# Kernel tuning notes

Measured on AMD Instinct MI355X. Metric: run time of the kernel, lower is better.

## Reference

```python
import jax, jax.numpy as jnp
import numpy as np

DEPTH = 4
CHUNK = 16


def tp(a, b):
    """Graded tensor (outer) product on flattened levels: (...,m)x(...,n)->(...,m*n)."""
    return jnp.einsum('...i,...j->...ij', a, b).reshape(*a.shape[:-1], a.shape[-1] * b.shape[-1])


def ta_mul(a, b):
    """Truncated tensor-algebra product of two group-like elements (implicit level-0 == 1).
    a, b: lists of levels 1..D, level k flattened to C**k."""
    out = []
    for k in range(len(a)):
        t = a[k] + b[k]
        for i in range(k):
            t = t + tp(a[i], b[k - 1 - i])
        out.append(t)
    return out


def ta_mulz(a, b):
    """Product when both elements have level-0 == 0."""
    out = []
    for k in range(len(a)):
        t = jnp.zeros_like(a[k])
        for i in range(k):
            t = t + tp(a[i], b[k - 1 - i])
        out.append(t)
    return out


def ta_exp(a):
    """exp of a level-0-free element, truncated at DEPTH; returns levels 1..D (level-0 == 1 implicit)."""
    out = list(a)
    p = a
    fact = 1.0
    for m in range(2, len(a) + 1):
        p = ta_mulz(a, p)
        fact *= m
        out = [o + q / fact for o, q in zip(out, p)]
    return out


def ta_log(s):
    """Truncated log of group-like element g = 1 + s; input s = levels 1..D of g."""
    out = list(s)
    p = s
    sign = 1.0
    for m in range(2, len(s) + 1):
        p = ta_mulz(s, p)
        sign = -sign
        out = [o + (sign / m) * q for o, q in zip(out, p)]
    return out


def bch(a, b):
    """BCH merge: log(exp(a) (x) exp(b)) in the truncated algebra."""
    return ta_log(ta_mul(ta_exp(a), ta_exp(b)))


def exp_l1(d):
    """exp of a pure level-1 element d (shape (...,C)): level k = d^(x)k / k!."""
    levels = [d]
    cur = d
    fact = 1.0
    for k in range(2, DEPTH + 1):
        cur = tp(cur, d)
        fact *= k
        levels.append(cur / fact)
    return levels


def chunk_signatures(inc):
    """inc: (B, N, L, C) per-chunk increments -> signature levels [(B,N,C), (B,N,C^2), ...]
    via Chen: sig = exp(d_1) (x) ... (x) exp(d_L)."""
    carry0 = tuple(exp_l1(inc[:, :, 0]))
    xs = jnp.moveaxis(inc[:, :, 1:], 2, 0)  # (L-1, B, N, C)
    def step(carry, d):
        return tuple(ta_mul(list(carry), exp_l1(d))), None
    carry, _ = jax.lax.scan(step, carry0, xs)
    return list(carry)


def hillis_steele(levels):
    """Inclusive associative scan over chunk dim (axis=1) with BCH merge.
    bch(0, b) == b exactly, so zero-padding handles the boundary."""
    N = levels[0].shape[1]
    pref = levels
    d = 1
    while d < N:
        shifted = [jnp.concatenate([jnp.zeros_like(l[:, :d]), l[:, :-d]], axis=1) for l in pref]
        pref = bch(shifted, pref)
        d *= 2
    return pref


def _forward(x, W1, b1, W2, b2):
    B, T, Cin = x.shape
    t = jnp.linspace(0.0, 1.0, T, dtype=x.dtype)
    path = jnp.concatenate([x, jnp.broadcast_to(t[None, :, None], (B, T, 1)).astype(x.dtype)], axis=-1)
    C = Cin + 1
    # basepoint=True: path starts at 0, so increments are diff of [0; path]
    inc = jnp.diff(path, axis=1, prepend=jnp.zeros((B, 1, C), x.dtype))
    N = T // CHUNK
    inc = inc.reshape(B, N, CHUNK, C)
    sig = chunk_signatures(inc)          # levels 1..D, (B,N,C^k)
    logl = ta_log(sig)                   # truncated log-signature per chunk
    pref = hillis_steele(logl)           # inclusive BCH prefix scan
    flat = jnp.concatenate(pref, axis=-1)  # (B, N, mem_dim)
    pooled = flat.mean(axis=1)           # readout_pool == 'mean'
    h = jnp.maximum(pooled @ W1 + b1, 0.0)
    return h @ W2 + b2


def setup_inputs() -> dict:
    key = jax.random.key(0)
    k0, k1, k2 = jax.random.split(key, 3)
    B, T, Cin = 8, 2048, 7
    mem_dim, H, out_dim = 4680, 256, 1
    x = jax.random.normal(k0, (B, T, Cin), dtype=jnp.float32)
    W1 = jax.random.normal(k1, (mem_dim, H), dtype=jnp.float32) * (1.0 / np.sqrt(mem_dim))
    b1 = jnp.zeros((H,), jnp.float32)
    W2 = jax.random.normal(k2, (H, out_dim), dtype=jnp.float32) * (1.0 / np.sqrt(H))
    b2 = jnp.zeros((out_dim,), jnp.float32)
    return {"x": x, "W1": W1, "b1": b1, "W2": W2, "b2": b2}


def reference(x, W1, b1, W2, b2):
    return _forward(x, W1, b1, W2, b2)
```

## Files before the change

### kernel.cpp

```cpp
#include <hip/hip_runtime.h>


#define MEM   4680
#define L2OFF 8
#define L3OFF 72
#define L4OFF 584
#define NG    32
#define TLEN  2048
#define ZN    (8 * MEM + 8 * 256)

__device__ __forceinline__ void load_inc(const float* __restrict__ x, int b, int g,
                                         float* sInc, int tid) {
    for (int e = tid; e < 512; e += 256) {
        int s = e >> 3, c = e & 7;
        int t = g * 64 + s;
        float v;
        if (c < 7) {
            float cur  = x[(b * TLEN + t) * 7 + c];
            float prev = (t > 0) ? x[(b * TLEN + t - 1) * 7 + c] : 0.f;
            v = cur - prev;
        } else v = (t > 0) ? (1.f / 2047.f) : 0.f;
        sInc[e] = v;
    }
}

__device__ __forceinline__ void chunk_step(const float* dch, float* sA, float* U, int tid) {
    float* loc3 = U;
    float* loc2 = U + 512;
    float* loc1 = U + 576;
    const int i1 = tid >> 6, j1 = (tid >> 3) & 7, k1 = tid & 7;
    const int pos2 = tid + 256, i2 = pos2 >> 6;
    float p1a = 0.f, l2a = 0.f, l3a = 0.f, p1b = 0.f, l2b = 0.f, l3b = 0.f;
    float Sa[8], Sb[8];
#pragma unroll
    for (int l = 0; l < 8; l++) { Sa[l] = 0.f; Sb[l] = 0.f; }
#pragma unroll
    for (int t = 0; t < 16; t++) {
        const float* dr = dch + t * 8;
        float di1 = dr[i1], di2 = dr[i2], dj = dr[j1], dk = dr[k1];
        float ga = l3a + dk * (l2a * 0.5f + dj * (p1a * (1.f/6.f) + di1 * (1.f/24.f)));
        float gb = l3b + dk * (l2b * 0.5f + dj * (p1b * (1.f/6.f) + di2 * (1.f/24.f)));
#pragma unroll
        for (int l = 0; l < 8; l++) { float dv = dr[l]; Sa[l] += ga * dv; Sb[l] += gb * dv; }
        l3a += dk * (l2a + dj * (p1a * 0.5f + di1 * (1.f/6.f)));
        l3b += dk * (l2b + dj * (p1b * 0.5f + di2 * (1.f/6.f)));
        l2a += (p1a + di1 * 0.5f) * dj;
        l2b += (p1b + di2 * 0.5f) * dj;
        p1a += di1; p1b += di2;
    }
    loc3[tid] = l3a; loc3[pos2] = l3b;
    if (k1 == 0) { loc2[tid >> 3] = l2a; loc2[(tid >> 3) + 32] = l2b; }
    if ((tid & 63) == 0) { loc1[i1] = p1a; loc1[i2] = p1b; }
    __syncthreads();
    float n4a[8], n4b[8];
    {
        float a1 = sA[i1], a2 = sA[L2OFF + (tid >> 3)], a3 = sA[L3OFF + tid];
        float c1_ = sA[i2], c2_ = sA[L2OFF + (tid >> 3) + 32], c3_ = sA[L3OFF + pos2];
        const float* l3p = &loc3[(tid & 63) * 8];
        const float* l2p = &loc2[k1 * 8];
#pragma unroll
        for (int l = 0; l < 8; l++) {
            float v3 = l3p[l], v2 = l2p[l], v1 = loc1[l];
            n4a[l] = sA[L4OFF + tid * 8 + l]  + Sa[l] + a1 * v3 + a2 * v2 + a3 * v1;
            n4b[l] = sA[L4OFF + pos2 * 8 + l] + Sb[l] + c1_ * v3 + c2_ * v2 + c3_ * v1;
        }
    }
    float n3a = sA[L3OFF + tid]  + l3a + sA[i1] * loc2[tid & 63] + sA[L2OFF + (tid >> 3)] * loc1[k1];
    float n3b = sA[L3OFF + pos2] + l3b + sA[i2] * loc2[tid & 63] + sA[L2OFF + (tid >> 3) + 32] * loc1[k1];
    float n2v = 0.f, n1v = 0.f;
    if (tid < 64) n2v = sA[L2OFF + tid] + loc2[tid] + sA[tid >> 3] * loc1[tid & 7];
    if (tid < 8)  n1v = sA[tid] + loc1[tid];
    __syncthreads();
#pragma unroll
    for (int l = 0; l < 8; l++) { sA[L4OFF + tid * 8 + l] = n4a[l]; sA[L4OFF + pos2 * 8 + l] = n4b[l]; }
    sA[L3OFF + tid] = n3a; sA[L3OFF + pos2] = n3b;
    if (tid < 64) sA[L2OFF + tid] = n2v;
    if (tid < 8)  sA[tid] = n1v;
    __syncthreads();
}

__global__ __launch_bounds__(256) void sig_totals_kernel(const float* __restrict__ x,
                                                         float* __restrict__ T,
                                                         float* __restrict__ zbuf) {
    int blk = blockIdx.x;
    int b = blk >> 5, g = blk & 31;
    int tid = threadIdx.x;

    for (int i = blk * 256 + tid; i < ZN; i += 256 * 256) zbuf[i] = 0.f;

    __shared__ __attribute__((aligned(16))) float sInc[512];
    __shared__ __attribute__((aligned(16))) float sA[MEM];
    __shared__ __attribute__((aligned(16))) float U[584];

    load_inc(x, b, g, sInc, tid);
    for (int m = tid; m < MEM; m += 256) sA[m] = 0.f;
    __syncthreads();
    for (int c = 0; c < 4; c++) chunk_step(&sInc[c * 128], sA, U, tid);
    const float4* s4 = (const float4*)sA;
    float4* t4 = (float4*)(T + (size_t)blk * MEM);
    for (int m = tid; m < MEM / 4; m += 256) t4[m] = s4[m];
}

__global__ __launch_bounds__(256) void scan_fused_kernel(const float* __restrict__ T,
                                                         float* __restrict__ P) {
    int bx = blockIdx.x;
    int b = bx >> 4, s = bx & 15;
    int tid = threadIdx.x;

    __shared__ float st1[NG][8];
    __shared__ float st2[NG][64];
    __shared__ float st3[NG][32];
    __shared__ float sp1[NG][8];
    __shared__ float sp2[NG][64];
    __shared__ float sp3[NG][32];

    int bBase = b * NG;
    {
        int g = tid >> 3, i = tid & 7;
        st1[g][i] = T[(size_t)(bBase + g) * MEM + i];
    }
    for (int m = tid; m < NG * 64; m += 256) {
        int g = m >> 6, e = m & 63;
        st2[g][e] = T[(size_t)(bBase + g) * MEM + L2OFF + e];
    }
    for (int m = tid; m < NG * 32; m += 256) {
        int g = m >> 5, e = m & 31;
        st3[g][e] = T[(size_t)(bBase + g) * MEM + L3OFF + s * 32 + e];
    }
    __syncthreads();

    if (tid < 64) {
        int i = tid >> 3, k = tid & 7;
        float p1acc = 0.f, p2acc = 0.f;
        for (int g = 0; g < NG; g++) {
            sp2[g][tid] = p2acc;
            if (k == 0) sp1[g][i] = p1acc;
            if (s == 0) {
                size_t prow = (size_t)(bBase + g) * MEM;
                P[prow + L2OFF + tid] = p2acc;
                if (k == 0) P[prow + i] = p1acc;
            }
            p2acc += st2[g][tid] + p1acc * st1[g][k];
            p1acc += st1[g][i];
        }
    }
    __syncthreads();
    if (tid < 32) {
        int ijk = s * 32 + tid;
        int i = ijk >> 6, jk = ijk & 63, ij = ijk >> 3, k = ijk & 7;
        float acc3 = 0.f;
        for (int g = 0; g < NG; g++) {
            sp3[g][tid] = acc3;
            P[(size_t)(bBase + g) * MEM + L3OFF + ijk] = acc3;
            acc3 += st3[g][tid] + sp1[g][i] * st2[g][jk] + sp2[g][ij] * st1[g][k];
        }
    }
    __syncthreads();
    {
        int m = s * 256 + tid;
        int i = m >> 9, jkl = m & 511, ij = m >> 6, kl = m & 63, l = m & 7;
        int p3loc = tid >> 3;
        float acc4 = 0.f;
#pragma unroll 4
        for (int g = 0; g < NG; g++) {
            size_t row = (size_t)(bBase + g) * MEM;
            P[row + L4OFF + m] = acc4;
            acc4 += T[row + L4OFF + m]
                  + sp1[g][i] * T[row + L3OFF + jkl]
                  + sp2[g][ij] * st2[g][kl]
                  + sp3[g][p3loc] * st1[g][l];
        }
    }
}

__global__ __launch_bounds__(256) void apply_log_pool_kernel(const float* __restrict__ x,
                                                             const float* __restrict__ P,
                                                             float* __restrict__ pooled) {
    int blk = blockIdx.x;
    int b = blk >> 5, g = blk & 31;
    int tid = threadIdx.x;

    __shared__ __attribute__((aligned(16))) float sInc[512];
    __shared__ __attribute__((aligned(16))) float sA[MEM];
    __shared__ __attribute__((aligned(16))) float sP[MEM];
    __shared__ __attribute__((aligned(16))) float U[1680];

    load_inc(x, b, g, sInc, tid);
    {
        const float4* p4 = (const float4*)(P + (size_t)blk * MEM);
        float4* sp4 = (float4*)sP;
        for (int m = tid; m < MEM / 4; m += 256) sp4[m] = p4[m];
    }
    for (int m = tid; m < MEM; m += 256) sA[m] = 0.f;
    __syncthreads();

    const int i1 = tid >> 6, j1 = (tid >> 3) & 7, k1 = tid & 7;
    const int pos2 = tid + 256, i2 = pos2 >> 6;
    float pool4a[8], pool4b[8];
#pragma unroll
    for (int l = 0; l < 8; l++) { pool4a[l] = 0.f; pool4b[l] = 0.f; }
    float pool3a = 0.f, pool3b = 0.f, pool2 = 0.f, pool1 = 0.f;
    float* sR = U + 584;
    float* sQ23 = U + 1168;

    for (int c = 0; c < 4; c++) {
        chunk_step(&sInc[c * 128], sA, U, tid);
        float R4a[8], R4b[8];
        {
            float a1 = sP[i1], a2 = sP[L2OFF + (tid >> 3)], a3 = sP[L3OFF + tid];
            float c1_ = sP[i2], c2_ = sP[L2OFF + (tid >> 3) + 32], c3_ = sP[L3OFF + pos2];
            const float* q3p = &sA[L3OFF + (tid & 63) * 8];
            const float* q2p = &sA[L2OFF + k1 * 8];
#pragma unroll
            for (int l = 0; l < 8; l++) {
                float v3 = q3p[l], v2 = q2p[l], v1 = sA[l];
                R4a[l] = sP[L4OFF + tid * 8 + l]  + sA[L4OFF + tid * 8 + l]  + a1 * v3 + a2 * v2 + a3 * v1;
                R4b[l] = sP[L4OFF + pos2 * 8 + l] + sA[L4OFF + pos2 * 8 + l] + c1_ * v3 + c2_ * v2 + c3_ * v1;
            }
        }
        float R3a = sP[L3OFF + tid]  + sA[L3OFF + tid]  + sP[i1] * sA[L2OFF + (tid & 63)] + sP[L2OFF + (tid >> 3)] * sA[k1];
        float R3b = sP[L3OFF + pos2] + sA[L3OFF + pos2] + sP[i2] * sA[L2OFF + (tid & 63)] + sP[L2OFF + (tid >> 3) + 32] * sA[k1];
        float R2v = 0.f, R1v = 0.f;
        if (tid < 64) R2v = sP[L2OFF + tid] + sA[L2OFF + tid] + sP[tid >> 3] * sA[tid & 7];
        if (tid < 8)  R1v = sP[tid] + sA[tid];
        sR[72 + tid] = R3a; sR[72 + pos2] = R3b;
        if (tid < 64) sR[8 + tid] = R2v;
        if (tid < 8)  sR[tid] = R1v;
        __syncthreads();
        sQ23[tid]  = sR[tid >> 6] * sR[8 + (tid & 63)] + sR[8 + (tid >> 3)] * sR[tid & 7];
        sQ23[pos2] = sR[pos2 >> 6] * sR[8 + (tid & 63)] + sR[8 + (tid >> 3) + 32] * sR[tid & 7];
        __syncthreads();
        {
            float s1ia = sR[i1], s1ib = sR[i2], s1j = sR[j1], s1k = sR[k1];
            float s2ija = sR[8 + (tid >> 3)], s2ijb = sR[8 + (tid >> 3) + 32];
            const float* r3p = &sR[72 + (tid & 63) * 8];
            const float* r2p = &sR[8 + k1 * 8];
            const float* q23p = &sQ23[(tid & 63) * 8];
#pragma unroll
            for (int l = 0; l < 8; l++) {
                float s1l = sR[l];
                float p22 = s1k * s1l;
                float p24a = s1ia * r3p[l] + s2ija * r2p[l] + R3a * s1l;
                float p24b = s1ib * r3p[l] + s2ijb * r2p[l] + R3b * s1l;
                float p34a = s1ia * q23p[l] + s2ija * p22;
                float p34b = s1ib * q23p[l] + s2ijb * p22;
                float p44a = s1ia * s1j * p22;
                float p44b = s1ib * s1j * p22;
                pool4a[l] += R4a[l] - 0.5f * p24a + (1.f/3.f) * p34a - 0.25f * p44a;
                pool4b[l] += R4b[l] - 0.5f * p24b + (1.f/3.f) * p34b - 0.25f * p44b;
            }
            pool3a += R3a - 0.5f * sQ23[tid]  + (1.f/3.f) * s1ia * s1j * s1k;
            pool3b += R3b - 0.5f * sQ23[pos2] + (1.f/3.f) * s1ib * s1j * s1k;
            if (tid < 64) pool2 += R2v - 0.5f * sR[tid >> 3] * sR[tid & 7];
            if (tid < 8)  pool1 += R1v;
        }
        __syncthreads();
    }
    {
        const float sc = 1.f / 128.f;
        float* pb = pooled + (size_t)b * MEM;
#pragma unroll
        for (int l = 0; l < 8; l++) {
            atomicAdd(&pb[L4OFF + tid * 8 + l],  pool4a[l] * sc);
            atomicAdd(&pb[L4OFF + pos2 * 8 + l], pool4b[l] * sc);
        }
        atomicAdd(&pb[L3OFF + tid],  pool3a * sc);
        atomicAdd(&pb[L3OFF + pos2], pool3b * sc);
        if (tid < 64) atomicAdd(&pb[L2OFF + tid], pool2 * sc);
        if (tid < 8)  atomicAdd(&pb[tid], pool1 * sc);
    }
}

__global__ __launch_bounds__(256) void gemv1_kernel(const float* __restrict__ pooled,
                                                    const float* __restrict__ W1,
                                                    float* __restrict__ hbuf) {
    int kc = blockIdx.x;
    int tid = threadIdx.x;
    int k0 = kc * 32;
    __shared__ float sp[8][32];
    {
        int b = tid >> 5, kk = tid & 31;
        sp[b][kk] = (k0 + kk < MEM) ? pooled[b * MEM + k0 + kk] : 0.f;
    }
    __syncthreads();
    float acc[8];
#pragma unroll
    for (int b = 0; b < 8; b++) acc[b] = 0.f;
    int kend = (k0 + 32 < MEM) ? (k0 + 32) : MEM;
    for (int k = k0; k < kend; k++) {
        float wv = W1[(size_t)k * 256 + tid];
#pragma unroll
        for (int b = 0; b < 8; b++) acc[b] += sp[b][k - k0] * wv;
    }
#pragma unroll
    for (int b = 0; b < 8; b++) atomicAdd(&hbuf[b * 256 + tid], acc[b]);
}

__global__ __launch_bounds__(256) void final_kernel(const float* __restrict__ hbuf,
                                                    const float* __restrict__ b1,
                                                    const float* __restrict__ W2,
                                                    const float* __restrict__ b2,
                                                    float* __restrict__ outp) {
    int b = blockIdx.x;
    int tid = threadIdx.x;
    float v = hbuf[b * 256 + tid] + b1[tid];
    v = fmaxf(v, 0.f) * W2[tid];
    __shared__ float sRed[256];
    sRed[tid] = v;
    __syncthreads();
    for (int s = 128; s > 0; s >>= 1) {
        if (tid < s) sRed[tid] += sRed[tid + s];
        __syncthreads();
    }
    if (tid == 0) outp[b] = sRed[0] + b2[0];
}

extern "C" void kernel_launch(void* const* d_in, const int* in_sizes, int n_in,
                              void* d_out, int out_size, void* d_ws, size_t ws_size,
                              hipStream_t stream) {
    const float* x  = (const float*)d_in[0];
    const float* W1 = (const float*)d_in[1];
    const float* b1 = (const float*)d_in[2];
    const float* W2 = (const float*)d_in[3];
    const float* b2 = (const float*)d_in[4];
    float* out = (float*)d_out;

    float* ws = (float*)d_ws;
    float* T      = ws;
    float* P      = T + (size_t)256 * MEM;
    float* pooled = P + (size_t)256 * MEM;
    float* hbuf   = pooled + 8 * MEM;

    sig_totals_kernel<<<256, 256, 0, stream>>>(x, T, pooled);
    scan_fused_kernel<<<128, 256, 0, stream>>>(T, P);
    apply_log_pool_kernel<<<256, 256, 0, stream>>>(x, P, pooled);
    gemv1_kernel<<<147, 256, 0, stream>>>(pooled, W1, hbuf);
    final_kernel<<<8, 256, 0, stream>>>(hbuf, b1, W2, b2, out);
}
```

Baseline: 152.0 us.

## Pad shared-memory signature rows to stride 9 and replace atomics with partial-sum buffers

Level-3 and level-4 tensors in shared memory are stored with a row stride of 9 instead of 8, so the strided per-thread accesses no longer hit the same LDS banks. The pooled reduction and the hidden-layer reduction now write per-block partial buffers, which the next kernel sums, instead of using global atomicAdd. This also removes the zero-initialisation pass. In exchange the code does extra global traffic: the 256x4680 partial buffer is read by gemv1 and 147 partial slices are summed in final_kernel. Shared memory per block also grows.

```diff
diff --git a/kernel.cpp b/kernel.cpp
--- a/kernel.cpp
+++ b/kernel.cpp
@@ -2,12 +2,12 @@
 
 
 #define MEM   4680
-#define L2OFF 8
-#define L3OFF 72
-#define L4OFF 584
 #define NG    32
 #define TLEN  2048
-#define ZN    (8 * MEM + 8 * 256)
+
+#define P3OFF 72
+#define P4OFF 648
+#define SIGSZ 5256
 
 __device__ __forceinline__ void load_inc(const float* __restrict__ x, int b, int g,
                                          float* sInc, int tid) {
@@ -26,9 +26,11 @@
 
 __device__ __forceinline__ void chunk_step(const float* dch, float* sA, float* U, int tid) {
     float* loc3 = U;
-    float* loc2 = U + 512;
-    float* loc1 = U + 576;
+    float* loc2 = U + 576;
+    float* loc1 = U + 640;
     const int i1 = tid >> 6, j1 = (tid >> 3) & 7, k1 = tid & 7;
+    const int row1 = tid >> 3, row2 = row1 + 32;
+    const int jk = tid & 63;
     const int pos2 = tid + 256, i2 = pos2 >> 6;
     float p1a = 0.f, l2a = 0.f, l3a = 0.f, p1b = 0.f, l2b = 0.f, l3b = 0.f;
     float Sa[8], Sb[8];
@@ -48,57 +50,60 @@
         l2b += (p1b + di2 * 0.5f) * dj;
         p1a += di1; p1b += di2;
     }
-    loc3[tid] = l3a; loc3[pos2] = l3b;
-    if (k1 == 0) { loc2[tid >> 3] = l2a; loc2[(tid >> 3) + 32] = l2b; }
-    if ((tid & 63) == 0) { loc1[i1] = p1a; loc1[i2] = p1b; }
-    __syncthreads();
+    loc3[row1 * 9 + k1] = l3a;
+    loc3[row2 * 9 + k1] = l3b;
+    if (k1 == 0) { loc2[row1] = l2a; loc2[row2] = l2b; }
+    if (jk == 0) { loc1[i1] = p1a; loc1[i2] = p1b; }
+    __syncthreads();
+    float a1 = sA[i1], a2 = sA[8 + row1], a3 = sA[P3OFF + row1 * 9 + k1];
+    float c1_ = sA[i2], c2_ = sA[8 + row2], c3_ = sA[P3OFF + row2 * 9 + k1];
+    const float* l3p = &loc3[jk * 9];
+    const float* l2p = &loc2[k1 * 8];
     float n4a[8], n4b[8];
-    {
-        float a1 = sA[i1], a2 = sA[L2OFF + (tid >> 3)], a3 = sA[L3OFF + tid];
-        float c1_ = sA[i2], c2_ = sA[L2OFF + (tid >> 3) + 32], c3_ = sA[L3OFF + pos2];
-        const float* l3p = &loc3[(tid & 63) * 8];
-        const float* l2p = &loc2[k1 * 8];
-#pragma unroll
-        for (int l = 0; l < 8; l++) {
-            float v3 = l3p[l], v2 = l2p[l], v1 = loc1[l];
-            n4a[l] = sA[L4OFF + tid * 8 + l]  + Sa[l] + a1 * v3 + a2 * v2 + a3 * v1;
-            n4b[l] = sA[L4OFF + pos2 * 8 + l] + Sb[l] + c1_ * v3 + c2_ * v2 + c3_ * v1;
-        }
-    }
-    float n3a = sA[L3OFF + tid]  + l3a + sA[i1] * loc2[tid & 63] + sA[L2OFF + (tid >> 3)] * loc1[k1];
-    float n3b = sA[L3OFF + pos2] + l3b + sA[i2] * loc2[tid & 63] + sA[L2OFF + (tid >> 3) + 32] * loc1[k1];
+#pragma unroll
+    for (int l = 0; l < 8; l++) {
+        float v3 = l3p[l], v2 = l2p[l], v1 = loc1[l];
+        n4a[l] = sA[P4OFF + tid * 9 + l]  + Sa[l] + a1 * v3 + a2 * v2 + a3 * v1;
+        n4b[l] = sA[P4OFF + pos2 * 9 + l] + Sb[l] + c1_ * v3 + c2_ * v2 + c3_ * v1;
+    }
+    float n3a = a3 + l3a + a1 * loc2[jk] + a2 * loc1[k1];
+    float n3b = c3_ + l3b + c1_ * loc2[jk] + c2_ * loc1[k1];
     float n2v = 0.f, n1v = 0.f;
-    if (tid < 64) n2v = sA[L2OFF + tid] + loc2[tid] + sA[tid >> 3] * loc1[tid & 7];
+    if (tid < 64) n2v = sA[8 + tid] + loc2[tid] + sA[tid >> 3] * loc1[tid & 7];
     if (tid < 8)  n1v = sA[tid] + loc1[tid];
     __syncthreads();
 #pragma unroll
-    for (int l = 0; l < 8; l++) { sA[L4OFF + tid * 8 + l] = n4a[l]; sA[L4OFF + pos2 * 8 + l] = n4b[l]; }
-    sA[L3OFF + tid] = n3a; sA[L3OFF + pos2] = n3b;
-    if (tid < 64) sA[L2OFF + tid] = n2v;
+    for (int l = 0; l < 8; l++) { sA[P4OFF + tid * 9 + l] = n4a[l]; sA[P4OFF + pos2 * 9 + l] = n4b[l]; }
+    sA[P3OFF + row1 * 9 + k1] = n3a;
+    sA[P3OFF + row2 * 9 + k1] = n3b;
+    if (tid < 64) sA[8 + tid] = n2v;
     if (tid < 8)  sA[tid] = n1v;
     __syncthreads();
 }
 
 __global__ __launch_bounds__(256) void sig_totals_kernel(const float* __restrict__ x,
-                                                         float* __restrict__ T,
-                                                         float* __restrict__ zbuf) {
+                                                         float* __restrict__ T) {
     int blk = blockIdx.x;
     int b = blk >> 5, g = blk & 31;
     int tid = threadIdx.x;
 
-    for (int i = blk * 256 + tid; i < ZN; i += 256 * 256) zbuf[i] = 0.f;
-
     __shared__ __attribute__((aligned(16))) float sInc[512];
-    __shared__ __attribute__((aligned(16))) float sA[MEM];
-    __shared__ __attribute__((aligned(16))) float U[584];
+    __shared__ __attribute__((aligned(16))) float sA[SIGSZ];
+    __shared__ __attribute__((aligned(16))) float U[648];
 
     load_inc(x, b, g, sInc, tid);
-    for (int m = tid; m < MEM; m += 256) sA[m] = 0.f;
+    for (int m = tid; m < SIGSZ; m += 256) sA[m] = 0.f;
     __syncthreads();
     for (int c = 0; c < 4; c++) chunk_step(&sInc[c * 128], sA, U, tid);
-    const float4* s4 = (const float4*)sA;
-    float4* t4 = (float4*)(T + (size_t)blk * MEM);
-    for (int m = tid; m < MEM / 4; m += 256) t4[m] = s4[m];
+
+    size_t base = (size_t)blk * MEM;
+    for (int m = tid; m < MEM; m += 256) {
+        float v;
+        if (m < 72) v = sA[m];
+        else if (m < 584) { int e = m - 72;  v = sA[P3OFF + (e >> 3) * 9 + (e & 7)]; }
+        else              { int e = m - 584; v = sA[P4OFF + (e >> 3) * 9 + (e & 7)]; }
+        T[base + m] = v;
+    }
 }
 
 __global__ __launch_bounds__(256) void scan_fused_kernel(const float* __restrict__ T,
@@ -121,11 +126,11 @@
     }
     for (int m = tid; m < NG * 64; m += 256) {
         int g = m >> 6, e = m & 63;
-        st2[g][e] = T[(size_t)(bBase + g) * MEM + L2OFF + e];
+        st2[g][e] = T[(size_t)(bBase + g) * MEM + 8 + e];
     }
     for (int m = tid; m < NG * 32; m += 256) {
         int g = m >> 5, e = m & 31;
-        st3[g][e] = T[(size_t)(bBase + g) * MEM + L3OFF + s * 32 + e];
+        st3[g][e] = T[(size_t)(bBase + g) * MEM + 72 + s * 32 + e];
     }
     __syncthreads();
 
@@ -137,7 +142,7 @@
             if (k == 0) sp1[g][i] = p1acc;
             if (s == 0) {
                 size_t prow = (size_t)(bBase + g) * MEM;
-                P[prow + L2OFF + tid] = p2acc;
+                P[prow + 8 + tid] = p2acc;
                 if (k == 0) P[prow + i] = p1acc;
             }
             p2acc += st2[g][tid] + p1acc * st1[g][k];
@@ -151,7 +156,7 @@
         float acc3 = 0.f;
         for (int g = 0; g < NG; g++) {
             sp3[g][tid] = acc3;
-            P[(size_t)(bBase + g) * MEM + L3OFF + ijk] = acc3;
+            P[(size_t)(bBase + g) * MEM + 72 + ijk] = acc3;
             acc3 += st3[g][tid] + sp1[g][i] * st2[g][jk] + sp2[g][ij] * st1[g][k];
         }
     }
@@ -164,9 +169,9 @@
 #pragma unroll 4
         for (int g = 0; g < NG; g++) {
             size_t row = (size_t)(bBase + g) * MEM;
-            P[row + L4OFF + m] = acc4;
-            acc4 += T[row + L4OFF + m]
-                  + sp1[g][i] * T[row + L3OFF + jkl]
+            P[row + 584 + m] = acc4;
+            acc4 += T[row + 584 + m]
+                  + sp1[g][i] * T[row + 72 + jkl]
                   + sp2[g][ij] * st2[g][kl]
                   + sp3[g][p3loc] * st1[g][l];
         }
@@ -175,67 +180,78 @@
 
 __global__ __launch_bounds__(256) void apply_log_pool_kernel(const float* __restrict__ x,
                                                              const float* __restrict__ P,
-                                                             float* __restrict__ pooled) {
+                                                             float* __restrict__ partial) {
     int blk = blockIdx.x;
     int b = blk >> 5, g = blk & 31;
     int tid = threadIdx.x;
 
     __shared__ __attribute__((aligned(16))) float sInc[512];
-    __shared__ __attribute__((aligned(16))) float sA[MEM];
-    __shared__ __attribute__((aligned(16))) float sP[MEM];
-    __shared__ __attribute__((aligned(16))) float U[1680];
+    __shared__ __attribute__((aligned(16))) float sA[SIGSZ];
+    __shared__ __attribute__((aligned(16))) float sP[SIGSZ];
+    __shared__ __attribute__((aligned(16))) float U[648];
+    __shared__ __attribute__((aligned(16))) float sR[648];
+    __shared__ __attribute__((aligned(16))) float sQ23[576];
 
     load_inc(x, b, g, sInc, tid);
     {
-        const float4* p4 = (const float4*)(P + (size_t)blk * MEM);
-        float4* sp4 = (float4*)sP;
-        for (int m = tid; m < MEM / 4; m += 256) sp4[m] = p4[m];
-    }
-    for (int m = tid; m < MEM; m += 256) sA[m] = 0.f;
+        size_t base = (size_t)blk * MEM;
+        if (tid < 72) sP[tid] = P[base + tid];
+        for (int e = tid; e < 512; e += 256)
+            sP[P3OFF + (e >> 3) * 9 + (e & 7)] = P[base + 72 + e];
+        for (int e = tid; e < 4096; e += 256)
+            sP[P4OFF + (e >> 3) * 9 + (e & 7)] = P[base + 584 + e];
+    }
+    for (int m = tid; m < SIGSZ; m += 256) sA[m] = 0.f;
     __syncthreads();
 
     const int i1 = tid >> 6, j1 = (tid >> 3) & 7, k1 = tid & 7;
+    const int row1 = tid >> 3, row2 = row1 + 32;
+    const int jk = tid & 63;
     const int pos2 = tid + 256, i2 = pos2 >> 6;
+
     float pool4a[8], pool4b[8];
 #pragma unroll
     for (int l = 0; l < 8; l++) { pool4a[l] = 0.f; pool4b[l] = 0.f; }
     float pool3a = 0.f, pool3b = 0.f, pool2 = 0.f, pool1 = 0.f;
-    float* sR = U + 584;
-    float* sQ23 = U + 1168;
 
     for (int c = 0; c < 4; c++) {
         chunk_step(&sInc[c * 128], sA, U, tid);
+
+        float a1 = sP[i1], a2 = sP[8 + row1], a3 = sP[P3OFF + row1 * 9 + k1];
+        float c1_ = sP[i2], c2_ = sP[8 + row2], c3_ = sP[P3OFF + row2 * 9 + k1];
+        const float* q3p = &sA[P3OFF + jk * 9];
+        const float* q2p = &sA[8 + k1 * 8];
         float R4a[8], R4b[8];
-        {
-            float a1 = sP[i1], a2 = sP[L2OFF + (tid >> 3)], a3 = sP[L3OFF + tid];
-            float c1_ = sP[i2], c2_ = sP[L2OFF + (tid >> 3) + 32], c3_ = sP[L3OFF + pos2];
-            const float* q3p = &sA[L3OFF + (tid & 63) * 8];
-            const float* q2p = &sA[L2OFF + k1 * 8];
-#pragma unroll
-            for (int l = 0; l < 8; l++) {
-                float v3 = q3p[l], v2 = q2p[l], v1 = sA[l];
-                R4a[l] = sP[L4OFF + tid * 8 + l]  + sA[L4OFF + tid * 8 + l]  + a1 * v3 + a2 * v2 + a3 * v1;
-                R4b[l] = sP[L4OFF + pos2 * 8 + l] + sA[L4OFF + pos2 * 8 + l] + c1_ * v3 + c2_ * v2 + c3_ * v1;
-            }
-        }
-        float R3a = sP[L3OFF + tid]  + sA[L3OFF + tid]  + sP[i1] * sA[L2OFF + (tid & 63)] + sP[L2OFF + (tid >> 3)] * sA[k1];
-        float R3b = sP[L3OFF + pos2] + sA[L3OFF + pos2] + sP[i2] * sA[L2OFF + (tid & 63)] + sP[L2OFF + (tid >> 3) + 32] * sA[k1];
+#pragma unroll
+        for (int l = 0; l < 8; l++) {
+            float v3 = q3p[l], v2 = q2p[l], v1 = sA[l];
+            R4a[l] = sP[P4OFF + tid * 9 + l]  + sA[P4OFF + tid * 9 + l]  + a1 * v3 + a2 * v2 + a3 * v1;
+            R4b[l] = sP[P4OFF + pos2 * 9 + l] + sA[P4OFF + pos2 * 9 + l] + c1_ * v3 + c2_ * v2 + c3_ * v1;
+        }
+        float R3a = a3 + sA[P3OFF + row1 * 9 + k1] + a1 * sA[8 + jk] + a2 * sA[k1];
+        float R3b = c3_ + sA[P3OFF + row2 * 9 + k1] + c1_ * sA[8 + jk] + c2_ * sA[k1];
         float R2v = 0.f, R1v = 0.f;
-        if (tid < 64) R2v = sP[L2OFF + tid] + sA[L2OFF + tid] + sP[tid >> 3] * sA[tid & 7];
+        if (tid < 64) R2v = sP[8 + tid] + sA[8 + tid] + sP[tid >> 3] * sA[tid & 7];
         if (tid < 8)  R1v = sP[tid] + sA[tid];
-        sR[72 + tid] = R3a; sR[72 + pos2] = R3b;
+
+        sR[P3OFF + row1 * 9 + k1] = R3a;
+        sR[P3OFF + row2 * 9 + k1] = R3b;
         if (tid < 64) sR[8 + tid] = R2v;
         if (tid < 8)  sR[tid] = R1v;
         __syncthreads();
-        sQ23[tid]  = sR[tid >> 6] * sR[8 + (tid & 63)] + sR[8 + (tid >> 3)] * sR[tid & 7];
-        sQ23[pos2] = sR[pos2 >> 6] * sR[8 + (tid & 63)] + sR[8 + (tid >> 3) + 32] * sR[tid & 7];
+
+        float q23a = sR[i1] * sR[8 + jk] + sR[8 + row1] * sR[k1];
+        float q23b = sR[i2] * sR[8 + jk] + sR[8 + row2] * sR[k1];
+        sQ23[row1 * 9 + k1] = q23a;
+        sQ23[row2 * 9 + k1] = q23b;
         __syncthreads();
+
         {
             float s1ia = sR[i1], s1ib = sR[i2], s1j = sR[j1], s1k = sR[k1];
-            float s2ija = sR[8 + (tid >> 3)], s2ijb = sR[8 + (tid >> 3) + 32];
-            const float* r3p = &sR[72 + (tid & 63) * 8];
+            float s2ija = sR[8 + row1], s2ijb = sR[8 + row2];
+            const float* r3p = &sR[P3OFF + jk * 9];
             const float* r2p = &sR[8 + k1 * 8];
-            const float* q23p = &sQ23[(tid & 63) * 8];
+            const float* q23p = &sQ23[jk * 9];
 #pragma unroll
             for (int l = 0; l < 8; l++) {
                 float s1l = sR[l];
@@ -249,61 +265,71 @@
                 pool4a[l] += R4a[l] - 0.5f * p24a + (1.f/3.f) * p34a - 0.25f * p44a;
                 pool4b[l] += R4b[l] - 0.5f * p24b + (1.f/3.f) * p34b - 0.25f * p44b;
             }
-            pool3a += R3a - 0.5f * sQ23[tid]  + (1.f/3.f) * s1ia * s1j * s1k;
-            pool3b += R3b - 0.5f * sQ23[pos2] + (1.f/3.f) * s1ib * s1j * s1k;
+            pool3a += R3a - 0.5f * q23a + (1.f/3.f) * s1ia * s1j * s1k;
+            pool3b += R3b - 0.5f * q23b + (1.f/3.f) * s1ib * s1j * s1k;
             if (tid < 64) pool2 += R2v - 0.5f * sR[tid >> 3] * sR[tid & 7];
             if (tid < 8)  pool1 += R1v;
         }
         __syncthreads();
     }
-    {
-        const float sc = 1.f / 128.f;
-        float* pb = pooled + (size_t)b * MEM;
-#pragma unroll
-        for (int l = 0; l < 8; l++) {
-            atomicAdd(&pb[L4OFF + tid * 8 + l],  pool4a[l] * sc);
-            atomicAdd(&pb[L4OFF + pos2 * 8 + l], pool4b[l] * sc);
-        }
-        atomicAdd(&pb[L3OFF + tid],  pool3a * sc);
-        atomicAdd(&pb[L3OFF + pos2], pool3b * sc);
-        if (tid < 64) atomicAdd(&pb[L2OFF + tid], pool2 * sc);
-        if (tid < 8)  atomicAdd(&pb[tid], pool1 * sc);
-    }
-}
-
-__global__ __launch_bounds__(256) void gemv1_kernel(const float* __restrict__ pooled,
+
+    {
+        float* pb = partial + (size_t)blk * MEM;
+        float4 va0 = make_float4(pool4a[0], pool4a[1], pool4a[2], pool4a[3]);
+        float4 va1 = make_float4(pool4a[4], pool4a[5], pool4a[6], pool4a[7]);
+        float4 vb0 = make_float4(pool4b[0], pool4b[1], pool4b[2], pool4b[3]);
+        float4 vb1 = make_float4(pool4b[4], pool4b[5], pool4b[6], pool4b[7]);
+        float4* d1 = (float4*)(pb + 584 + tid * 8);
+        d1[0] = va0; d1[1] = va1;
+        float4* d2 = (float4*)(pb + 584 + (tid + 256) * 8);
+        d2[0] = vb0; d2[1] = vb1;
+        pb[72 + tid] = pool3a;
+        pb[72 + tid + 256] = pool3b;
+        if (tid < 64) pb[8 + tid] = pool2;
+        if (tid < 8)  pb[tid] = pool1;
+    }
+}
+
+__global__ __launch_bounds__(256) void gemv1_kernel(const float* __restrict__ partial,
                                                     const float* __restrict__ W1,
-                                                    float* __restrict__ hbuf) {
+                                                    float* __restrict__ hpart) {
     int kc = blockIdx.x;
     int tid = threadIdx.x;
     int k0 = kc * 32;
     __shared__ float sp[8][32];
     {
-        int b = tid >> 5, kk = tid & 31;
-        sp[b][kk] = (k0 + kk < MEM) ? pooled[b * MEM + k0 + kk] : 0.f;
+        int b = tid >> 5, k = tid & 31;
+        float sum = 0.f;
+        if (k0 + k < MEM) {
+            for (int g = 0; g < NG; g++)
+                sum += partial[(size_t)(b * NG + g) * MEM + k0 + k];
+        }
+        sp[b][k] = sum * (1.f / 128.f);
     }
     __syncthreads();
     float acc[8];
 #pragma unroll
     for (int b = 0; b < 8; b++) acc[b] = 0.f;
-    int kend = (k0 + 32 < MEM) ? (k0 + 32) : MEM;
-    for (int k = k0; k < kend; k++) {
-        float wv = W1[(size_t)k * 256 + tid];
-#pragma unroll
-        for (int b = 0; b < 8; b++) acc[b] += sp[b][k - k0] * wv;
-    }
-#pragma unroll
-    for (int b = 0; b < 8; b++) atomicAdd(&hbuf[b * 256 + tid], acc[b]);
-}
-
-__global__ __launch_bounds__(256) void final_kernel(const float* __restrict__ hbuf,
+    int kend = (k0 + 32 < MEM) ? 32 : (MEM - k0);
+    for (int k = 0; k < kend; k++) {
+        float wv = W1[(size_t)(k0 + k) * 256 + tid];
+#pragma unroll
+        for (int b = 0; b < 8; b++) acc[b] += sp[b][k] * wv;
+    }
+#pragma unroll
+    for (int b = 0; b < 8; b++) hpart[(size_t)kc * 2048 + b * 256 + tid] = acc[b];
+}
+
+__global__ __launch_bounds__(256) void final_kernel(const float* __restrict__ hpart,
                                                     const float* __restrict__ b1,
                                                     const float* __restrict__ W2,
                                                     const float* __restrict__ b2,
                                                     float* __restrict__ outp) {
     int b = blockIdx.x;
     int tid = threadIdx.x;
-    float v = hbuf[b * 256 + tid] + b1[tid];
+    float v = 0.f;
+    for (int kc = 0; kc < 147; kc++) v += hpart[(size_t)kc * 2048 + b * 256 + tid];
+    v += b1[tid];
     v = fmaxf(v, 0.f) * W2[tid];
     __shared__ float sRed[256];
     sRed[tid] = v;
@@ -326,14 +352,14 @@
     float* out = (float*)d_out;
 
     float* ws = (float*)d_ws;
-    float* T      = ws;
-    float* P      = T + (size_t)256 * MEM;
-    float* pooled = P + (size_t)256 * MEM;
-    float* hbuf   = pooled + 8 * MEM;
-
-    sig_totals_kernel<<<256, 256, 0, stream>>>(x, T, pooled);
+    float* T       = ws;
+    float* P       = T + (size_t)256 * MEM;
+    float* partial = P + (size_t)256 * MEM;
+    float* hpart   = partial + (size_t)256 * MEM;
+
+    sig_totals_kernel<<<256, 256, 0, stream>>>(x, T);
     scan_fused_kernel<<<128, 256, 0, stream>>>(T, P);
-    apply_log_pool_kernel<<<256, 256, 0, stream>>>(x, P, pooled);
-    gemv1_kernel<<<147, 256, 0, stream>>>(pooled, W1, hbuf);
-    final_kernel<<<8, 256, 0, stream>>>(hbuf, b1, W2, b2, out);
-}
+    apply_log_pool_kernel<<<256, 256, 0, stream>>>(x, P, partial);
+    gemv1_kernel<<<147, 256, 0, stream>>>(partial, W1, hpart);
+    final_kernel<<<8, 256, 0, stream>>>(hpart, b1, W2, b2, out);
+}
```

After: 126.8 us. 16.6% less time.
